# Optimization experiments

Measured on AMD Instinct MI355X. Metric: run time of the kernel, lower is better.

The kernel has to match this reference:

```python
import jax, jax.numpy as jnp
import numpy as np

MAX_DEG = 10  # deepchem GraphConv default max_deg
EPS = 1e-5


def _neighbor_sum(h, adj, deg):
    # h: [B,N,F], adj: [B,N,K] padded neighbor indices, deg: [B,N]
    B = h.shape[0]
    g = h[jnp.arange(B)[:, None, None], adj]  # [B,N,K,F] irregular gather
    mask = (jnp.arange(MAX_DEG)[None, None, :] < deg[:, :, None]).astype(h.dtype)
    return jnp.einsum('bnkf,bnk->bnf', g, mask)


def _graph_conv(h, adj, deg, W_neigh, W_self, b_neigh, b_self):
    # Degree-bucketed conv: atoms of degree d use W_self[d] (and W_neigh[d-1] if d>=1)
    ns = _neighbor_sum(h, adj, deg)  # [B,N,F]
    out = jnp.zeros(h.shape[:-1] + (W_self.shape[-1],), h.dtype)
    for d in range(MAX_DEG + 1):
        m = (deg == d)[..., None].astype(h.dtype)
        t = h @ W_self[d] + b_self[d]
        if d >= 1:
            t = t + ns @ W_neigh[d - 1] + b_neigh[d - 1]
        out = out + m * t
    return out


def _batch_norm(h, gamma, beta):
    # training-mode batch norm over (batch, atom) for each feature channel
    mu = jnp.mean(h, axis=(0, 1), keepdims=True)
    var = jnp.var(h, axis=(0, 1), keepdims=True)
    return (h - mu) * jax.lax.rsqrt(var + EPS) * gamma + beta


def setup_inputs() -> dict:
    key = jax.random.key(0)
    ks = jax.random.split(key, 12)
    B, N, F, H, T = 128, 512, 75, 128, 12
    x = jax.random.normal(ks[0], (B, N, F), dtype=jnp.float32)
    adjacency_list = jax.random.randint(ks[1], (B, N, MAX_DEG), 0, N)
    degree_list = jax.random.randint(ks[2], (B, N), 0, MAX_DEG + 1)
    s1 = 1.0 / np.sqrt(F)
    s2 = 1.0 / np.sqrt(H)
    return {
        'x': x,
        'adjacency_list': adjacency_list,
        'degree_list': degree_list,
        'W_neigh1': jax.random.normal(ks[3], (MAX_DEG, F, H), dtype=jnp.float32) * s1,
        'W_self1': jax.random.normal(ks[4], (MAX_DEG + 1, F, H), dtype=jnp.float32) * s1,
        'b_neigh1': jnp.zeros((MAX_DEG, H), jnp.float32),
        'b_self1': jnp.zeros((MAX_DEG + 1, H), jnp.float32),
        'gamma1': jnp.ones((H,), jnp.float32),
        'beta1': jnp.zeros((H,), jnp.float32),
        'W_neigh2': jax.random.normal(ks[5], (MAX_DEG, H, H), dtype=jnp.float32) * s2,
        'W_self2': jax.random.normal(ks[6], (MAX_DEG + 1, H, H), dtype=jnp.float32) * s2,
        'b_neigh2': jnp.zeros((MAX_DEG, H), jnp.float32),
        'b_self2': jnp.zeros((MAX_DEG + 1, H), jnp.float32),
        'gamma2': jnp.ones((H,), jnp.float32),
        'beta2': jnp.zeros((H,), jnp.float32),
        'W_dense': jax.random.normal(ks[7], (H, T), dtype=jnp.float32) * s2,
        'b_dense': jnp.zeros((T,), jnp.float32),
    }


def reference(x, adjacency_list, degree_list,
              W_neigh1, W_self1, b_neigh1, b_self1, gamma1, beta1,
              W_neigh2, W_self2, b_neigh2, b_self2, gamma2, beta2,
              W_dense, b_dense):
    h = _graph_conv(x, adjacency_list, degree_list, W_neigh1, W_self1, b_neigh1, b_self1)
    h = jax.nn.relu(_batch_norm(h, gamma1, beta1))
    h = _graph_conv(h, adjacency_list, degree_list, W_neigh2, W_self2, b_neigh2, b_self2)
    h = jax.nn.relu(_batch_norm(h, gamma2, beta2))
    # dropout is identity at inference
    h = jnp.mean(h, axis=1)  # graph-level mean pool over atoms -> [B,H]
    return h @ W_dense + b_dense  # [B, n_tasks]
```

## Files before the change

kernel.cpp:

```cpp
#include <hip/hip_runtime.h>

#define NODES   65536
#define NGRAPH  512
#define BATCH   128
#define HID     128
#define TOUT    12
#define MAXDEG  10
#define NDEG    11
#define EPSV    1e-5f
#define MT      128
#define MAXT    (NODES / MT)

typedef float f32x4 __attribute__((ext_vector_type(4)));

__device__ __forceinline__ f32x4 ntload(const float* p) {
    return __builtin_nontemporal_load((const f32x4*)p);
}
__device__ __forceinline__ void ntstore(float* p, f32x4 v) {
    __builtin_nontemporal_store(v, (f32x4*)p);
}

__global__ void k_zero(f32x4* part4, float* stats1, float* stats2, int* cnt) {
    int i = blockIdx.x * 256 + threadIdx.x;
    part4[i] = 0.f;
    if (blockIdx.x == 0) {
        stats1[threadIdx.x] = 0.f;
        stats2[threadIdx.x] = 0.f;
        if (threadIdx.x < 16) cnt[threadIdx.x] = 0;
    }
}

__global__ void k_bucket(const int* __restrict__ deg, int* __restrict__ cnt,
                         int* __restrict__ lists) {
    __shared__ int s_cnt[NDEG];
    __shared__ int s_base[NDEG];
    int t = threadIdx.x;
    if (t < NDEG) s_cnt[t] = 0;
    __syncthreads();
    int i = blockIdx.x * 256 + t;
    int d = deg[i];
    d = d < 0 ? 0 : (d > MAXDEG ? MAXDEG : d);
    int pos = atomicAdd(&s_cnt[d], 1);
    __syncthreads();
    if (t < NDEG) s_base[t] = atomicAdd(&cnt[t], s_cnt[t]);
    __syncthreads();
    lists[d * NODES + s_base[d] + pos] = i;
}

__global__ void k_build1(const float* __restrict__ Ws, const float* __restrict__ Wn,
                         float* __restrict__ Wcat) {
    int idx = blockIdx.x * 256 + threadIdx.x;
    int h4 = idx & 31;
    int k  = (idx >> 5) % 160;
    int d  = idx / (160 * 32);
    f32x4 v = 0.f;
    if (k < 75)
        v = *(const f32x4*)(Ws + ((size_t)d * 75 + k) * 128 + h4 * 4);
    else if (k >= 80 && k < 155 && d >= 1)
        v = *(const f32x4*)(Wn + ((size_t)(d - 1) * 75 + (k - 80)) * 128 + h4 * 4);
    *(f32x4*)(Wcat + ((size_t)d * 160 + k) * 128 + h4 * 4) = v;
}
__global__ void k_build2(const float* __restrict__ Ws, const float* __restrict__ Wn,
                         float* __restrict__ Wcat) {
    int idx = blockIdx.x * 256 + threadIdx.x;
    int h4 = idx & 31;
    int k  = (idx >> 5) & 255;
    int d  = idx >> 13;
    f32x4 v = 0.f;
    if (k < 128)
        v = *(const f32x4*)(Ws + ((size_t)d * 128 + k) * 128 + h4 * 4);
    else if (d >= 1)
        v = *(const f32x4*)(Wn + ((size_t)(d - 1) * 128 + (k - 128)) * 128 + h4 * 4);
    *(f32x4*)(Wcat + ((size_t)d * 256 + k) * 128 + h4 * 4) = v;
}
__global__ void k_bias(const float* bs1, const float* bn1, const float* bs2, const float* bn2,
                       float* bcat1, float* bcat2) {
    int d = blockIdx.x, t = threadIdx.x;
    if (t < 128) bcat1[d * 128 + t] = bs1[d * 128 + t] + (d > 0 ? bn1[(d - 1) * 128 + t] : 0.f);
    else { int h = t - 128; bcat2[d * 128 + h] = bs2[d * 128 + h] + (d > 0 ? bn2[(d - 1) * 128 + h] : 0.f); }
}

__global__ void k_ns1(const float* __restrict__ x, const int* __restrict__ adj,
                      const int* __restrict__ deg, float* __restrict__ feats1) {
    int idx = blockIdx.x * 256 + threadIdx.x;
    int node = idx / 20;
    int q = idx - node * 20;
    int f = q * 4;
    int d = deg[node];
    d = d < 0 ? 0 : (d > MAXDEG ? MAXDEG : d);
    const int* arow = adj + node * MAXDEG;
    int base = node & ~(NGRAPH - 1);
    f32x4 s = 0.f;
    for (int k = 0; k < d; ++k) {
        const float* xr = x + (size_t)(base + arow[k]) * 75 + f;
        if (f + 3 < 75) { s.x += xr[0]; s.y += xr[1]; s.z += xr[2]; s.w += xr[3]; }
        else {
            if (f + 0 < 75) s.x += xr[0];
            if (f + 1 < 75) s.y += xr[1];
            if (f + 2 < 75) s.z += xr[2];
        }
    }
    *(f32x4*)(feats1 + (size_t)node * 160 + 80 + f) = s;
    f32x4 v = 0.f;
    const float* xs = x + (size_t)node * 75 + f;
    if (f + 3 < 75) { v.x = xs[0]; v.y = xs[1]; v.z = xs[2]; v.w = xs[3]; }
    else {
        if (f + 0 < 75) v.x = xs[0];
        if (f + 1 < 75) v.y = xs[1];
        if (f + 2 < 75) v.z = xs[2];
    }
    *(f32x4*)(feats1 + (size_t)node * 160 + f) = v;
}

__global__ void k_ns2(const float* __restrict__ feats2r, const int* __restrict__ adj,
                      const int* __restrict__ deg, float* __restrict__ feats2w) {
    int idx = blockIdx.x * 256 + threadIdx.x;
    int node = idx >> 5;
    int f = (idx & 31) * 4;
    int d = deg[node];
    d = d < 0 ? 0 : (d > MAXDEG ? MAXDEG : d);
    const int* arow = adj + node * MAXDEG;
    int base = node & ~(NGRAPH - 1);
    f32x4 s = 0.f;
    for (int k = 0; k < d; ++k) {
        f32x4 v = *(const f32x4*)(feats2r + (size_t)(base + arow[k]) * 256 + f);
        s += v;
    }
    *(f32x4*)(feats2w + (size_t)node * 256 + 128 + f) = s;
}

template<int S, int OS>
__global__ __launch_bounds__(256, 4)
void k_conv(const float* __restrict__ feats, const float* __restrict__ Wcat,
            const float* __restrict__ bcat, const int* __restrict__ lists,
            const int* __restrict__ cnt, float* __restrict__ out,
            float* __restrict__ partials) {
    constexpr int NCH = S / 32;

    __shared__ int   s_ids[MT];
    __shared__ float sW[2][32][128];
    __shared__ float sF[2][32][128];

    const int d  = blockIdx.y;
    const int c  = cnt[d];
    const int m0 = blockIdx.x * MT;
    if (m0 >= c) return;
    const int mv = min(MT, c - m0);
    const int t  = threadIdx.x;

    if (t < MT) s_ids[t] = lists[d * NODES + m0 + (t < mv ? t : 0)];
    __syncthreads();

    const int kw = t >> 3;
    const int cw = (t & 7) * 16;
    const int rf = t >> 1;
    const int ks = (t & 1) * 16;
    const float* Wbase = Wcat + (size_t)d * S * 128;
    const float* Fbase = feats + (size_t)s_ids[rf] * S;

    f32x4 w0, w1, w2, w3, f0, f1, f2, f3;
    auto LOAD = [&](int ch) {
        const float* wp = Wbase + (size_t)(ch * 32 + kw) * 128 + cw;
        w0 = *(const f32x4*)(wp);      w1 = *(const f32x4*)(wp + 4);
        w2 = *(const f32x4*)(wp + 8);  w3 = *(const f32x4*)(wp + 12);
        const float* fp = Fbase + ch * 32 + ks;
        f0 = ntload(fp); f1 = ntload(fp + 4); f2 = ntload(fp + 8); f3 = ntload(fp + 12);
    };
    auto STORE = [&](int buf) {
        *(f32x4*)&sW[buf][kw][cw + 0]  = w0;
        *(f32x4*)&sW[buf][kw][cw + 4]  = w1;
        *(f32x4*)&sW[buf][kw][cw + 8]  = w2;
        *(f32x4*)&sW[buf][kw][cw + 12] = w3;
        sF[buf][ks +  0][rf] = f0.x; sF[buf][ks +  1][rf] = f0.y;
        sF[buf][ks +  2][rf] = f0.z; sF[buf][ks +  3][rf] = f0.w;
        sF[buf][ks +  4][rf] = f1.x; sF[buf][ks +  5][rf] = f1.y;
        sF[buf][ks +  6][rf] = f1.z; sF[buf][ks +  7][rf] = f1.w;
        sF[buf][ks +  8][rf] = f2.x; sF[buf][ks +  9][rf] = f2.y;
        sF[buf][ks + 10][rf] = f2.z; sF[buf][ks + 11][rf] = f2.w;
        sF[buf][ks + 12][rf] = f3.x; sF[buf][ks + 13][rf] = f3.y;
        sF[buf][ks + 14][rf] = f3.z; sF[buf][ks + 15][rf] = f3.w;
    };

    const int cg = t & 15;
    const int rg = t >> 4;

    f32x4 acc[8][2];
    {
        f32x4 b0 = *(const f32x4*)(bcat + d * HID + cg * 8);
        f32x4 b1 = *(const f32x4*)(bcat + d * HID + cg * 8 + 4);
        #pragma unroll
        for (int j = 0; j < 8; ++j) { acc[j][0] = b0; acc[j][1] = b1; }
    }

    LOAD(0); STORE(0);
    __syncthreads();

    for (int ch = 0; ch < NCH; ++ch) {
        const int buf = ch & 1;
        const bool more = (ch + 1 < NCH);
        if (more) LOAD(ch + 1);
        #pragma unroll 8
        for (int k = 0; k < 32; ++k) {
            f32x4 wA = *(const f32x4*)&sW[buf][k][cg * 8];
            f32x4 wB = *(const f32x4*)&sW[buf][k][cg * 8 + 4];
            f32x4 fA = *(const f32x4*)&sF[buf][k][rg * 8];
            f32x4 fB = *(const f32x4*)&sF[buf][k][rg * 8 + 4];
            acc[0][0] += fA.x * wA;  acc[0][1] += fA.x * wB;
            acc[1][0] += fA.y * wA;  acc[1][1] += fA.y * wB;
            acc[2][0] += fA.z * wA;  acc[2][1] += fA.z * wB;
            acc[3][0] += fA.w * wA;  acc[3][1] += fA.w * wB;
            acc[4][0] += fB.x * wA;  acc[4][1] += fB.x * wB;
            acc[5][0] += fB.y * wA;  acc[5][1] += fB.y * wB;
            acc[6][0] += fB.z * wA;  acc[6][1] += fB.z * wB;
            acc[7][0] += fB.w * wA;  acc[7][1] += fB.w * wB;
        }
        if (more) STORE(buf ^ 1);
        __syncthreads();
    }

    f32x4 cs0 = 0.f, cs1 = 0.f, cq0 = 0.f, cq1 = 0.f;
    #pragma unroll
    for (int j = 0; j < 8; ++j) {
        int i = rg * 8 + j;
        if (i < mv) {
            float* op = out + (size_t)s_ids[i] * OS + cg * 8;
            ntstore(op, acc[j][0]);
            ntstore(op + 4, acc[j][1]);
            cs0 += acc[j][0]; cs1 += acc[j][1];
            cq0 += acc[j][0] * acc[j][0]; cq1 += acc[j][1] * acc[j][1];
        }
    }
    __syncthreads();
    float* red = &sW[0][0][0];
    *(f32x4*)&red[rg * 256 + cg * 8]       = cs0;
    *(f32x4*)&red[rg * 256 + cg * 8 + 4]   = cs1;
    *(f32x4*)&red[rg * 256 + 128 + cg * 8]     = cq0;
    *(f32x4*)&red[rg * 256 + 128 + cg * 8 + 4] = cq1;
    __syncthreads();
    float tot = 0.f;
    #pragma unroll
    for (int g = 0; g < 16; ++g) tot += red[g * 256 + t];
    atomicAdd(&partials[(size_t)blockIdx.x * 256 + t], tot);
}

__global__ void k_redstats(float* __restrict__ partials, float* __restrict__ stats) {
    int t = threadIdx.x;
    float acc = 0.f;
    for (int bx = blockIdx.x; bx < MAXT; bx += gridDim.x) {
        float* p = partials + (size_t)bx * 256 + t;
        acc += *p;
        *p = 0.f;
    }
    atomicAdd(&stats[t], acc);
}

__global__ void k_bnrelu(float* __restrict__ feats2, const float* __restrict__ stats,
                         const float* __restrict__ gamma, const float* __restrict__ beta) {
    int idx = blockIdx.x * 256 + threadIdx.x;
    int node = idx >> 5;
    int c4 = (idx & 31) * 4;
    float* p = feats2 + (size_t)node * 256 + c4;
    f32x4 v = *(f32x4*)p;
    const float inv = 1.f / (float)NODES;
    #pragma unroll
    for (int j = 0; j < 4; ++j) {
        int col = c4 + j;
        float mu  = stats[col] * inv;
        float var = stats[HID + col] * inv - mu * mu;
        float rs  = rsqrtf(var + EPSV);
        float sc  = gamma[col] * rs;
        float sh  = beta[col] - mu * sc;
        v[j] = fmaxf(fmaf(v[j], sc, sh), 0.f);
    }
    *(f32x4*)p = v;
}

__global__ void k_pool_dense(const float* __restrict__ h2, const float* __restrict__ stats,
                             const float* __restrict__ gamma, const float* __restrict__ beta,
                             const float* __restrict__ Wd, const float* __restrict__ bd,
                             float* __restrict__ outp) {
    __shared__ float s_part[4][HID];
    __shared__ float s_pool[HID];
    const int b = blockIdx.x;
    const int t = threadIdx.x;
    const int hcol = t & (HID - 1);
    const int q = t >> 7;
    const float inv = 1.f / (float)NODES;
    float mu  = stats[hcol] * inv;
    float var = stats[HID + hcol] * inv - mu * mu;
    float rs  = rsqrtf(var + EPSV);
    float sc  = gamma[hcol] * rs;
    float sh  = beta[hcol] - mu * sc;
    float acc = 0.f;
    const float* hp = h2 + ((size_t)b * NGRAPH + q * 128) * HID + hcol;
    #pragma unroll 4
    for (int n = 0; n < 128; ++n)
        acc += fmaxf(fmaf(hp[(size_t)n * HID], sc, sh), 0.f);
    s_part[q][hcol] = acc;
    __syncthreads();
    if (t < HID)
        s_pool[t] = (s_part[0][t] + s_part[1][t] + s_part[2][t] + s_part[3][t]) * (1.f / NGRAPH);
    __syncthreads();
    if (t < TOUT) {
        float o = bd[t];
        for (int hh = 0; hh < HID; ++hh)
            o = fmaf(s_pool[hh], Wd[hh * TOUT + t], o);
        outp[b * TOUT + t] = o;
    }
}

extern "C" void kernel_launch(void* const* d_in, const int* in_sizes, int n_in,
                              void* d_out, int out_size, void* d_ws, size_t ws_size,
                              hipStream_t stream) {
    const float* x   = (const float*)d_in[0];
    const int*   adj = (const int*)d_in[1];
    const int*   deg = (const int*)d_in[2];
    const float* Wn1 = (const float*)d_in[3];
    const float* Ws1 = (const float*)d_in[4];
    const float* bn1 = (const float*)d_in[5];
    const float* bs1 = (const float*)d_in[6];
    const float* g1  = (const float*)d_in[7];
    const float* be1 = (const float*)d_in[8];
    const float* Wn2 = (const float*)d_in[9];
    const float* Ws2 = (const float*)d_in[10];
    const float* bn2 = (const float*)d_in[11];
    const float* bs2 = (const float*)d_in[12];
    const float* g2  = (const float*)d_in[13];
    const float* be2 = (const float*)d_in[14];
    const float* Wd  = (const float*)d_in[15];
    const float* bd  = (const float*)d_in[16];

    float* ws     = (float*)d_ws;
    float* feats1 = ws;
    float* h2     = ws;
    float* feats2 = ws + 10485760;
    float* Wcat1  = ws + 27262976;
    float* Wcat2  = ws + 27488256;
    float* bcat1  = ws + 27848704;
    float* bcat2  = ws + 27850112;
    float* part   = ws + 27851520;
    float* stats1 = ws + 27982592;
    float* stats2 = ws + 27982848;
    int*   cnt    = (int*)(ws + 27983104);
    int*   lists  = cnt + 16;

    k_zero<<<128, 256, 0, stream>>>((f32x4*)part, stats1, stats2, cnt);
    k_bucket<<<NODES / 256, 256, 0, stream>>>(deg, cnt, lists);
    k_build1<<<220, 256, 0, stream>>>(Ws1, Wn1, Wcat1);
    k_build2<<<352, 256, 0, stream>>>(Ws2, Wn2, Wcat2);
    k_bias<<<NDEG, 256, 0, stream>>>(bs1, bn1, bs2, bn2, bcat1, bcat2);

    k_ns1<<<NODES * 20 / 256, 256, 0, stream>>>(x, adj, deg, feats1);
    k_conv<160, 256><<<dim3(MAXT, NDEG), 256, 0, stream>>>(feats1, Wcat1, bcat1,
                                                           lists, cnt, feats2, part);
    k_redstats<<<32, 256, 0, stream>>>(part, stats1);
    k_bnrelu<<<8192, 256, 0, stream>>>(feats2, stats1, g1, be1);

    k_ns2<<<8192, 256, 0, stream>>>(feats2, adj, deg, feats2);
    k_conv<256, 128><<<dim3(MAXT, NDEG), 256, 0, stream>>>(feats2, Wcat2, bcat2,
                                                           lists, cnt, h2, part);
    k_redstats<<<32, 256, 0, stream>>>(part, stats2);

    k_pool_dense<<<BATCH, 512, 0, stream>>>(h2, stats2, g2, be2, Wd, bd, (float*)d_out);
}
```

Baseline: 375.4 us.

## Compact conv grid via per-degree tile offsets and use 512-thread blocks

Adds a small planning kernel that prefix-sums per-degree tile counts, so the conv kernels launch a flat grid of exactly the needed tiles instead of an 11x512 grid where most blocks exit at once. Each conv block now runs 512 threads, each computing 8 rows by 4 columns, which halves per-thread accumulators and is meant to raise occupancy. The feature tile in LDS is padded to reduce bank conflicts. Per-tile statistics are written with plain stores instead of atomics. The cost is an extra tiny launch and a serial dependency on the counts.

```diff
diff --git a/kernel.cpp b/kernel.cpp
--- a/kernel.cpp
+++ b/kernel.cpp
@@ -9,7 +9,8 @@
 #define NDEG    11
 #define EPSV    1e-5f
 #define MT      128
-#define MAXT    (NODES / MT)
+#define NTILES  (NODES / MT + NDEG)
+#define PCAP    544
 
 typedef float f32x4 __attribute__((ext_vector_type(4)));
 
@@ -45,6 +46,17 @@
     if (t < NDEG) s_base[t] = atomicAdd(&cnt[t], s_cnt[t]);
     __syncthreads();
     lists[d * NODES + s_base[d] + pos] = i;
+}
+
+__global__ void k_plan(const int* __restrict__ cnt, int* __restrict__ offs) {
+    if (threadIdx.x == 0) {
+        int acc = 0;
+        offs[0] = 0;
+        for (int d = 0; d < NDEG; ++d) {
+            acc += (cnt[d] + MT - 1) / MT;
+            offs[d + 1] = acc;
+        }
+    }
 }
 
 __global__ void k_build1(const float* __restrict__ Ws, const float* __restrict__ Wn,
@@ -130,66 +142,65 @@
 }
 
 template<int S, int OS>
-__global__ __launch_bounds__(256, 4)
+__global__ __launch_bounds__(512, 4)
 void k_conv(const float* __restrict__ feats, const float* __restrict__ Wcat,
             const float* __restrict__ bcat, const int* __restrict__ lists,
-            const int* __restrict__ cnt, float* __restrict__ out,
-            float* __restrict__ partials) {
+            const int* __restrict__ cnt, const int* __restrict__ offs,
+            float* __restrict__ out, float* __restrict__ partials) {
     constexpr int NCH = S / 32;
 
     __shared__ int   s_ids[MT];
     __shared__ float sW[2][32][128];
-    __shared__ float sF[2][32][128];
-
-    const int d  = blockIdx.y;
+    __shared__ float sF[2][32][132];
+
+    const int bid = blockIdx.x;
+    if (bid >= offs[NDEG]) return;
+    int d = 0;
+    #pragma unroll
+    for (int q = 1; q < NDEG; ++q) d += (bid >= offs[q]);
     const int c  = cnt[d];
-    const int m0 = blockIdx.x * MT;
-    if (m0 >= c) return;
+    const int m0 = (bid - offs[d]) * MT;
     const int mv = min(MT, c - m0);
     const int t  = threadIdx.x;
 
     if (t < MT) s_ids[t] = lists[d * NODES + m0 + (t < mv ? t : 0)];
     __syncthreads();
 
-    const int kw = t >> 3;
-    const int cw = (t & 7) * 16;
-    const int rf = t >> 1;
-    const int ks = (t & 1) * 16;
+    const int kw = t >> 5;
+    const int c4 = t & 31;
+    const int fr = t >> 3;
+    const int kq = t & 7;
     const float* Wbase = Wcat + (size_t)d * S * 128;
-    const float* Fbase = feats + (size_t)s_ids[rf] * S;
-
-    f32x4 w0, w1, w2, w3, f0, f1, f2, f3;
+    const float* Fb0 = feats + (size_t)s_ids[fr] * S;
+    const float* Fb1 = feats + (size_t)s_ids[fr + 64] * S;
+
+    f32x4 w0, w1, f0, f1;
     auto LOAD = [&](int ch) {
-        const float* wp = Wbase + (size_t)(ch * 32 + kw) * 128 + cw;
-        w0 = *(const f32x4*)(wp);      w1 = *(const f32x4*)(wp + 4);
-        w2 = *(const f32x4*)(wp + 8);  w3 = *(const f32x4*)(wp + 12);
-        const float* fp = Fbase + ch * 32 + ks;
-        f0 = ntload(fp); f1 = ntload(fp + 4); f2 = ntload(fp + 8); f3 = ntload(fp + 12);
+        const float* wp = Wbase + (size_t)(ch * 32 + kw) * 128 + c4 * 4;
+        w0 = *(const f32x4*)(wp);
+        w1 = *(const f32x4*)(wp + 16 * 128);
+        const float* fp0 = Fb0 + ch * 32 + kq * 4;
+        const float* fp1 = Fb1 + ch * 32 + kq * 4;
+        f0 = ntload(fp0);
+        f1 = ntload(fp1);
     };
     auto STORE = [&](int buf) {
-        *(f32x4*)&sW[buf][kw][cw + 0]  = w0;
-        *(f32x4*)&sW[buf][kw][cw + 4]  = w1;
-        *(f32x4*)&sW[buf][kw][cw + 8]  = w2;
-        *(f32x4*)&sW[buf][kw][cw + 12] = w3;
-        sF[buf][ks +  0][rf] = f0.x; sF[buf][ks +  1][rf] = f0.y;
-        sF[buf][ks +  2][rf] = f0.z; sF[buf][ks +  3][rf] = f0.w;
-        sF[buf][ks +  4][rf] = f1.x; sF[buf][ks +  5][rf] = f1.y;
-        sF[buf][ks +  6][rf] = f1.z; sF[buf][ks +  7][rf] = f1.w;
-        sF[buf][ks +  8][rf] = f2.x; sF[buf][ks +  9][rf] = f2.y;
-        sF[buf][ks + 10][rf] = f2.z; sF[buf][ks + 11][rf] = f2.w;
-        sF[buf][ks + 12][rf] = f3.x; sF[buf][ks + 13][rf] = f3.y;
-        sF[buf][ks + 14][rf] = f3.z; sF[buf][ks + 15][rf] = f3.w;
+        *(f32x4*)&sW[buf][kw][c4 * 4]      = w0;
+        *(f32x4*)&sW[buf][kw + 16][c4 * 4] = w1;
+        sF[buf][kq * 4 + 0][fr] = f0.x; sF[buf][kq * 4 + 1][fr] = f0.y;
+        sF[buf][kq * 4 + 2][fr] = f0.z; sF[buf][kq * 4 + 3][fr] = f0.w;
+        sF[buf][kq * 4 + 0][fr + 64] = f1.x; sF[buf][kq * 4 + 1][fr + 64] = f1.y;
+        sF[buf][kq * 4 + 2][fr + 64] = f1.z; sF[buf][kq * 4 + 3][fr + 64] = f1.w;
     };
 
-    const int cg = t & 15;
-    const int rg = t >> 4;
-
-    f32x4 acc[8][2];
+    const int cg = t & 31;
+    const int rg = t >> 5;
+
+    f32x4 acc[8];
     {
-        f32x4 b0 = *(const f32x4*)(bcat + d * HID + cg * 8);
-        f32x4 b1 = *(const f32x4*)(bcat + d * HID + cg * 8 + 4);
+        f32x4 b = *(const f32x4*)(bcat + d * HID + cg * 4);
         #pragma unroll
-        for (int j = 0; j < 8; ++j) { acc[j][0] = b0; acc[j][1] = b1; }
+        for (int j = 0; j < 8; ++j) acc[j] = b;
     }
 
     LOAD(0); STORE(0);
@@ -201,52 +212,49 @@
         if (more) LOAD(ch + 1);
         #pragma unroll 8
         for (int k = 0; k < 32; ++k) {
-            f32x4 wA = *(const f32x4*)&sW[buf][k][cg * 8];
-            f32x4 wB = *(const f32x4*)&sW[buf][k][cg * 8 + 4];
+            f32x4 wv = *(const f32x4*)&sW[buf][k][cg * 4];
             f32x4 fA = *(const f32x4*)&sF[buf][k][rg * 8];
             f32x4 fB = *(const f32x4*)&sF[buf][k][rg * 8 + 4];
-            acc[0][0] += fA.x * wA;  acc[0][1] += fA.x * wB;
-            acc[1][0] += fA.y * wA;  acc[1][1] += fA.y * wB;
-            acc[2][0] += fA.z * wA;  acc[2][1] += fA.z * wB;
-            acc[3][0] += fA.w * wA;  acc[3][1] += fA.w * wB;
-            acc[4][0] += fB.x * wA;  acc[4][1] += fB.x * wB;
-            acc[5][0] += fB.y * wA;  acc[5][1] += fB.y * wB;
-            acc[6][0] += fB.z * wA;  acc[6][1] += fB.z * wB;
-            acc[7][0] += fB.w * wA;  acc[7][1] += fB.w * wB;
+            acc[0] += fA.x * wv;
+            acc[1] += fA.y * wv;
+            acc[2] += fA.z * wv;
+            acc[3] += fA.w * wv;
+            acc[4] += fB.x * wv;
+            acc[5] += fB.y * wv;
+            acc[6] += fB.z * wv;
+            acc[7] += fB.w * wv;
         }
         if (more) STORE(buf ^ 1);
         __syncthreads();
     }
 
-    f32x4 cs0 = 0.f, cs1 = 0.f, cq0 = 0.f, cq1 = 0.f;
+    f32x4 cs = 0.f, cq = 0.f;
     #pragma unroll
     for (int j = 0; j < 8; ++j) {
         int i = rg * 8 + j;
         if (i < mv) {
-            float* op = out + (size_t)s_ids[i] * OS + cg * 8;
-            ntstore(op, acc[j][0]);
-            ntstore(op + 4, acc[j][1]);
-            cs0 += acc[j][0]; cs1 += acc[j][1];
-            cq0 += acc[j][0] * acc[j][0]; cq1 += acc[j][1] * acc[j][1];
+            ntstore(out + (size_t)s_ids[i] * OS + cg * 4, acc[j]);
+            cs += acc[j];
+            cq += acc[j] * acc[j];
         }
     }
     __syncthreads();
     float* red = &sW[0][0][0];
-    *(f32x4*)&red[rg * 256 + cg * 8]       = cs0;
-    *(f32x4*)&red[rg * 256 + cg * 8 + 4]   = cs1;
-    *(f32x4*)&red[rg * 256 + 128 + cg * 8]     = cq0;
-    *(f32x4*)&red[rg * 256 + 128 + cg * 8 + 4] = cq1;
-    __syncthreads();
-    float tot = 0.f;
-    #pragma unroll
-    for (int g = 0; g < 16; ++g) tot += red[g * 256 + t];
-    atomicAdd(&partials[(size_t)blockIdx.x * 256 + t], tot);
+    *(f32x4*)&red[rg * 256 + cg * 4]       = cs;
+    *(f32x4*)&red[rg * 256 + 128 + cg * 4] = cq;
+    __syncthreads();
+    if (t < 256) {
+        float tot = 0.f;
+        #pragma unroll
+        for (int g = 0; g < 16; ++g) tot += red[g * 256 + t];
+        partials[(size_t)bid * 256 + t] = tot;
+    }
 }
 
 __global__ void k_redstats(float* __restrict__ partials, float* __restrict__ stats) {
     int t = threadIdx.x;
     float acc = 0.f;
-    for (int bx = blockIdx.x; bx < MAXT; bx += gridDim.x) {
+    for (int bx = blockIdx.x; bx < PCAP; bx += gridDim.x) {
         float* p = partials + (size_t)bx * 256 + t;
         acc += *p;
         *p = 0.f;
@@ -339,26 +347,28 @@
     float* bcat1  = ws + 27848704;
     float* bcat2  = ws + 27850112;
     float* part   = ws + 27851520;
-    float* stats1 = ws + 27982592;
-    float* stats2 = ws + 27982848;
-    int*   cnt    = (int*)(ws + 27983104);
-    int*   lists  = cnt + 16;
-
-    k_zero<<<128, 256, 0, stream>>>((f32x4*)part, stats1, stats2, cnt);
+    float* stats1 = ws + 27990784;
+    float* stats2 = ws + 27991040;
+    int*   cnt    = (int*)(ws + 27991296);
+    int*   offs   = cnt + 16;
+    int*   lists  = cnt + 32;
+
+    k_zero<<<PCAP / 4, 256, 0, stream>>>((f32x4*)part, stats1, stats2, cnt);
     k_bucket<<<NODES / 256, 256, 0, stream>>>(deg, cnt, lists);
+    k_plan<<<1, 64, 0, stream>>>(cnt, offs);
     k_build1<<<220, 256, 0, stream>>>(Ws1, Wn1, Wcat1);
     k_build2<<<352, 256, 0, stream>>>(Ws2, Wn2, Wcat2);
     k_bias<<<NDEG, 256, 0, stream>>>(bs1, bn1, bs2, bn2, bcat1, bcat2);
 
     k_ns1<<<NODES * 20 / 256, 256, 0, stream>>>(x, adj, deg, feats1);
-    k_conv<160, 256><<<dim3(MAXT, NDEG), 256, 0, stream>>>(feats1, Wcat1, bcat1,
-                                                           lists, cnt, feats2, part);
+    k_conv<160, 256><<<NTILES, 512, 0, stream>>>(feats1, Wcat1, bcat1,
+                                                 lists, cnt, offs, feats2, part);
     k_redstats<<<32, 256, 0, stream>>>(part, stats1);
     k_bnrelu<<<8192, 256, 0, stream>>>(feats2, stats1, g1, be1);
 
     k_ns2<<<8192, 256, 0, stream>>>(feats2, adj, deg, feats2);
-    k_conv<256, 128><<<dim3(MAXT, NDEG), 256, 0, stream>>>(feats2, Wcat2, bcat2,
-                                                           lists, cnt, h2, part);
+    k_conv<256, 128><<<NTILES, 512, 0, stream>>>(feats2, Wcat2, bcat2,
+                                                 lists, cnt, offs, h2, part);
     k_redstats<<<32, 256, 0, stream>>>(part, stats2);
 
     k_pool_dense<<<BATCH, 512, 0, stream>>>(h2, stats2, g2, be2, Wd, bd, (float*)d_out);
```

Measured after the change: 357.0 us. 1.05x faster.
